# Optimization experiments

Hardware: AMD Instinct MI355X
Metric: run time of the kernel (lower is better)

The kernel has to match this reference:

```python
import jax, jax.numpy as jnp
import numpy as np

H, W = 1024, 2048
PS, ST = 16, 8          # patch_size, stride (init kwargs)
MARGIN = 1e-4           # margin from nerfstudio depth_ranking_loss
NH = (H - PS) // ST + 1  # 127
NW = (W - PS) // ST + 1  # 255
P = NH * NW             # 32385 patches
N = PS * PS             # 256 pixels per patch


def setup_inputs() -> dict:
    key = jax.random.key(0)
    k1, k2, k3, k4 = jax.random.split(key, 4)
    pred = jax.random.normal(k1, (1, 1, H, W), dtype=jnp.float32)
    target = jax.random.normal(k2, (1, 1, H, W), dtype=jnp.float32)
    mask = jax.random.bernoulli(k3, 0.5, (1, 1, H, W))
    # per-patch randomness standing in for torch.randperm: argsort of this
    # noise restricted to valid pixels is a uniform random permutation of
    # the masked (valid) pixel list.
    perm_noise = jax.random.uniform(k4, (P, N), dtype=jnp.float32)
    return {"pred": pred, "target": target, "mask": mask, "perm_noise": perm_noise}


def _extract_patches(x):
    # x: [H, W] -> [P, N] overlapping PSxPS patches with stride ST (scan order)
    i0 = jnp.arange(0, H - PS + 1, ST)           # [NH]
    j0 = jnp.arange(0, W - PS + 1, ST)           # [NW]
    ii = i0[:, None] + jnp.arange(PS)[None, :]   # [NH, PS]
    jj = j0[:, None] + jnp.arange(PS)[None, :]   # [NW, PS]
    g = x[ii[:, None, :, None], jj[None, :, None, :]]  # [NH, NW, PS, PS]
    return g.reshape(P, N)


def reference(pred, target, mask, perm_noise):
    pp = _extract_patches(pred[0, 0])            # [P, N]
    tp = _extract_patches(target[0, 0])          # [P, N]
    mp = _extract_patches(mask[0, 0])            # [P, N] bool

    # rank of each valid pixel in scan order (torch: pred_patch[mask] ordering)
    rank = jnp.cumsum(mp.astype(jnp.int32), axis=1) - 1        # [P, N]
    # random permutation of valid pixels: valid pixels sorted by noise come first
    noise = jnp.where(mp, perm_noise, jnp.inf)
    order = jnp.argsort(noise, axis=1)                          # [P, N]
    # valid pixel with scan-rank r pairs with order[r] (a random valid pixel)
    partner = jnp.take_along_axis(order, jnp.clip(rank, 0, N - 1), axis=1)

    dt = tp - jnp.take_along_axis(tp, partner, axis=1)
    dp = pp - jnp.take_along_axis(pp, partner, axis=1) + MARGIN

    # depth_ranking_loss: penalize pairs whose signs disagree, loss = mean |dp|
    sel = mp & (jnp.sign(dt) != jnp.sign(dp))
    cnt = jnp.sum(sel, axis=1).astype(pp.dtype)                 # [P]
    patch_loss = jnp.sum(jnp.where(sel, jnp.abs(dp), 0.0), axis=1) / cnt

    has_valid = jnp.any(mp, axis=1)                             # skip empty-mask patches
    n_used = jnp.sum(has_valid).astype(pp.dtype)
    return jnp.sum(jnp.where(has_valid, patch_loss, 0.0)) / n_used
```

## Files before the change

### kernel.cpp

```cpp
#include <hip/hip_runtime.h>
#include <cstdint>

#define H 1024
#define W 2048
#define PS 16
#define ST 8
#define NHH ((H - PS) / ST + 1)
#define NWW ((W - PS) / ST + 1)
#define NPATCH (NHH * NWW)
#define NN 256
#define MARGIN 1e-4f
#define WPB 4
#define NSLOT 128
#define SLOT_STRIDE 8

#define WS_VALID_F 1024

#define DPP_I(old, src, ctrl, rmask, bmask, bc) \
    __builtin_amdgcn_update_dpp((old), (src), (ctrl), (rmask), (bmask), (bc))

__device__ __forceinline__ unsigned wave_iscan_u32(unsigned x) {
    int v = (int)x;
    v += DPP_I(0, v, 0x111, 0xF, 0xF, true);
    v += DPP_I(0, v, 0x112, 0xF, 0xF, true);
    v += DPP_I(0, v, 0x114, 0xF, 0xF, true);
    v += DPP_I(0, v, 0x118, 0xF, 0xF, true);
    v += DPP_I(0, v, 0x142, 0xA, 0xF, true);
    v += DPP_I(0, v, 0x143, 0xC, 0xF, true);
    return (unsigned)v;
}

__device__ __forceinline__ float wave_iscan_f32(float x) {
    float v = x;
#define STEPF(ctrl, rmask) \
    v += __int_as_float(DPP_I(0, __float_as_int(v), (ctrl), (rmask), 0xF, true));
    STEPF(0x111, 0xF) STEPF(0x112, 0xF) STEPF(0x114, 0xF) STEPF(0x118, 0xF)
    STEPF(0x142, 0xA) STEPF(0x143, 0xC)
#undef STEPF
    return v;
}

__device__ __forceinline__ int rank_of(const unsigned* __restrict__ slot,
                                       unsigned w, unsigned key) {
    const unsigned b = w >> 16;
    const unsigned e = w & 0xFFFFu;
    const unsigned n = e - b;
    const unsigned v0 = slot[b + 0];
    const unsigned v1 = slot[b + 1];
    const unsigned v2 = slot[b + 2];
    const unsigned v3 = slot[b + 3];
    int rk = (int)b;
    rk += (n > 0u && v0 < key);
    rk += (n > 1u && v1 < key);
    rk += (n > 2u && v2 < key);
    rk += (n > 3u && v3 < key);
    if (__builtin_expect(n > 4u, 0)) {
        for (unsigned j = b + 4; j < e; ++j) rk += (slot[j] < key);
    }
    return rk;
}

__global__ __launch_bounds__(256, 8) void patch_loss_kernel(
    const float* __restrict__ pred, const float* __restrict__ target,
    const void* __restrict__ mask, const float* __restrict__ noise,
    float* __restrict__ lossAcc, float* __restrict__ validAcc)
{
    __shared__ unsigned sHist[WPB][NN];
    __shared__ unsigned sSlot[WPB][NN + 4];
    __shared__ float2   sPair[WPB][NN];

    const int tid  = threadIdx.x;
    const int lane = tid & 63;
    const int wid  = tid >> 6;
    const int p = blockIdx.x * WPB + wid;
    if (p >= NPATCH) return;

    const int ih = p / NWW;
    const int iw = p - ih * NWW;
    const int e0  = lane << 2;
    const int row = e0 >> 4;
    const int col = e0 & 15;
    const int pix = (ih * ST + row) * W + iw * ST + col;

    const float4 nz = *(const float4*)(noise + (size_t)p * NN + e0);

    const unsigned wb = *(const unsigned*)((const unsigned char*)mask + pix);
    int m0, m1, m2, m3;
    if (__ballot(wb > 1u) != 0ULL) {
        m0 = (wb & 0x000000FFu) != 0; m1 = (wb & 0x0000FF00u) != 0;
        m2 = (wb & 0x00FF0000u) != 0; m3 = (wb & 0xFF000000u) != 0;
    } else {
        const int4 mv = *(const int4*)((const int*)mask + pix);
        m0 = mv.x != 0; m1 = mv.y != 0; m2 = mv.z != 0; m3 = mv.w != 0;
    }

    const unsigned long long bl0 = __ballot(m0);
    const unsigned long long bl1 = __ballot(m1);
    const unsigned long long bl2 = __ballot(m2);
    const unsigned long long bl3 = __ballot(m3);
    const unsigned long long below = (1ULL << lane) - 1ULL;
    const int pre = __popcll(bl0 & below) + __popcll(bl1 & below)
                  + __popcll(bl2 & below) + __popcll(bl3 & below);
    const int cnt = __popcll(bl0) + __popcll(bl1)
                  + __popcll(bl2) + __popcll(bl3);
    const int r0 = pre;
    const int r1 = r0 + m0;
    const int r2 = r1 + m1;
    const int r3 = r2 + m2;

    const unsigned k0 = ((__float_as_uint(nz.x + 1.0f) - 0x3F800000u) << 8) | (unsigned)(e0 + 0);
    const unsigned k1 = ((__float_as_uint(nz.y + 1.0f) - 0x3F800000u) << 8) | (unsigned)(e0 + 1);
    const unsigned k2 = ((__float_as_uint(nz.z + 1.0f) - 0x3F800000u) << 8) | (unsigned)(e0 + 2);
    const unsigned k3 = ((__float_as_uint(nz.w + 1.0f) - 0x3F800000u) << 8) | (unsigned)(e0 + 3);

    *(uint4*)&sHist[wid][e0] = make_uint4(0u, 0u, 0u, 0u);
    __builtin_amdgcn_wave_barrier();
    if (m0) atomicAdd(&sHist[wid][k0 >> 23], 1u);
    if (m1) atomicAdd(&sHist[wid][k1 >> 23], 1u);
    if (m2) atomicAdd(&sHist[wid][k2 >> 23], 1u);
    if (m3) atomicAdd(&sHist[wid][k3 >> 23], 1u);
    __builtin_amdgcn_wave_barrier();

    const uint4 hq = *(uint4*)&sHist[wid][e0];
    const unsigned lsum = hq.x + hq.y + hq.z + hq.w;
    const unsigned hincl = wave_iscan_u32(lsum);
    const unsigned c0 = hincl - lsum;
    const unsigned c1 = c0 + hq.x;
    const unsigned c2 = c1 + hq.y;
    const unsigned c3 = c2 + hq.z;
    *(uint4*)&sHist[wid][e0] = make_uint4((c0 << 16) | c0, (c1 << 16) | c1,
                                          (c2 << 16) | c2, (c3 << 16) | c3);
    __builtin_amdgcn_wave_barrier();

    if (m0) { const unsigned s = atomicAdd(&sHist[wid][k0 >> 23], 1u) & 0xFFFFu; sSlot[wid][s] = k0; }
    if (m1) { const unsigned s = atomicAdd(&sHist[wid][k1 >> 23], 1u) & 0xFFFFu; sSlot[wid][s] = k1; }
    if (m2) { const unsigned s = atomicAdd(&sHist[wid][k2 >> 23], 1u) & 0xFFFFu; sSlot[wid][s] = k2; }
    if (m3) { const unsigned s = atomicAdd(&sHist[wid][k3 >> 23], 1u) & 0xFFFFu; sSlot[wid][s] = k3; }
    __builtin_amdgcn_wave_barrier();

    const float4 pv = *(const float4*)(pred + pix);
    const float4 tv = *(const float4*)(target + pix);

    const unsigned* __restrict__ slot  = sSlot[wid];
    const unsigned* __restrict__ histp = sHist[wid];
    const unsigned w0 = histp[k0 >> 23];
    const unsigned w1 = histp[k1 >> 23];
    const unsigned w2 = histp[k2 >> 23];
    const unsigned w3 = histp[k3 >> 23];
    const int rk0 = rank_of(slot, w0, k0);
    const int rk1 = rank_of(slot, w1, k1);
    const int rk2 = rank_of(slot, w2, k2);
    const int rk3 = rank_of(slot, w3, k3);

    if (m0) sPair[wid][rk0] = make_float2(tv.x, pv.x);
    if (m1) sPair[wid][rk1] = make_float2(tv.y, pv.y);
    if (m2) sPair[wid][rk2] = make_float2(tv.z, pv.z);
    if (m3) sPair[wid][rk3] = make_float2(tv.w, pv.w);
    __builtin_amdgcn_wave_barrier();

    const float2 q0 = sPair[wid][r0 & 255];
    const float2 q1 = sPair[wid][r1 & 255];
    const float2 q2 = sPair[wid][r2 & 255];
    const float2 q3 = sPair[wid][r3 & 255];

    float la = 0.0f;
    int   lc = 0;
    {
        const float dt = tv.x - q0.x, dp = pv.x - q0.y + MARGIN;
        const bool sel = m0 && (((dt > 0.0f) - (dt < 0.0f)) != ((dp > 0.0f) - (dp < 0.0f)));
        la += sel ? fabsf(dp) : 0.0f; lc += sel;
    }
    {
        const float dt = tv.y - q1.x, dp = pv.y - q1.y + MARGIN;
        const bool sel = m1 && (((dt > 0.0f) - (dt < 0.0f)) != ((dp > 0.0f) - (dp < 0.0f)));
        la += sel ? fabsf(dp) : 0.0f; lc += sel;
    }
    {
        const float dt = tv.z - q2.x, dp = pv.z - q2.y + MARGIN;
        const bool sel = m2 && (((dt > 0.0f) - (dt < 0.0f)) != ((dp > 0.0f) - (dp < 0.0f)));
        la += sel ? fabsf(dp) : 0.0f; lc += sel;
    }
    {
        const float dt = tv.w - q3.x, dp = pv.w - q3.y + MARGIN;
        const bool sel = m3 && (((dt > 0.0f) - (dt < 0.0f)) != ((dp > 0.0f) - (dp < 0.0f)));
        la += sel ? fabsf(dp) : 0.0f; lc += sel;
    }

    la = wave_iscan_f32(la);
    const unsigned lct = wave_iscan_u32((unsigned)lc);
    if (lane == 63 && cnt > 0) {
        const int slot_o = (p & (NSLOT - 1)) * SLOT_STRIDE;
        atomicAdd(&lossAcc[slot_o],  la / (float)lct);
        atomicAdd(&validAcc[slot_o], 1.0f);
    }
}

__global__ void finalize_kernel(const float* __restrict__ wsf,
                                float* __restrict__ out) {
    const int lane = threadIdx.x;
    float a = wsf[lane * SLOT_STRIDE] + wsf[(lane + 64) * SLOT_STRIDE];
    float b = wsf[WS_VALID_F + lane * SLOT_STRIDE]
            + wsf[WS_VALID_F + (lane + 64) * SLOT_STRIDE];
#pragma unroll
    for (int off = 32; off > 0; off >>= 1) {
        a += __shfl_down(a, off);
        b += __shfl_down(b, off);
    }
    if (lane == 0) out[0] = a / b;
}

extern "C" void kernel_launch(void* const* d_in, const int* in_sizes, int n_in,
                              void* d_out, int out_size, void* d_ws, size_t ws_size,
                              hipStream_t stream) {
    const float* pred   = (const float*)d_in[0];
    const float* target = (const float*)d_in[1];
    const void*  mask   = d_in[2];
    const float* noise  = (const float*)d_in[3];

    float* wsf      = (float*)d_ws;
    float* lossAcc  = wsf;
    float* validAcc = wsf + WS_VALID_F;

    const int nblocks = (NPATCH + WPB - 1) / WPB;
    patch_loss_kernel<<<nblocks, 256, 0, stream>>>(pred, target, mask, noise,
                                                   lossAcc, validAcc);
    finalize_kernel<<<1, 64, 0, stream>>>(wsf, (float*)d_out);
}
```

Before: 104.6 us.

## Invert pairing direction and use fixed-capacity bucket slots to drop a scatter pass

```diff
diff --git a/kernel.cpp b/kernel.cpp
--- a/kernel.cpp
+++ b/kernel.cpp
@@ -9,6 +9,8 @@
 #define NWW ((W - PS) / ST + 1)
 #define NPATCH (NHH * NWW)
 #define NN 256
+#define NBIN 256
+#define CAP 4
 #define MARGIN 1e-4f
 #define WPB 4
 #define NSLOT 128
@@ -40,33 +42,22 @@
     return v;
 }
 
-__device__ __forceinline__ int rank_of(const unsigned* __restrict__ slot,
-                                       unsigned w, unsigned key) {
-    const unsigned b = w >> 16;
-    const unsigned e = w & 0xFFFFu;
-    const unsigned n = e - b;
-    const unsigned v0 = slot[b + 0];
-    const unsigned v1 = slot[b + 1];
-    const unsigned v2 = slot[b + 2];
-    const unsigned v3 = slot[b + 3];
-    int rk = (int)b;
-    rk += (n > 0u && v0 < key);
-    rk += (n > 1u && v1 < key);
-    rk += (n > 2u && v2 < key);
-    rk += (n > 3u && v3 < key);
-    if (__builtin_expect(n > 4u, 0)) {
-        for (unsigned j = b + 4; j < e; ++j) rk += (slot[j] < key);
-    }
-    return rk;
-}
-
-__global__ __launch_bounds__(256, 8) void patch_loss_kernel(
+__device__ __forceinline__ int rank_in(uint4 c, unsigned n, unsigned key) {
+    int r = 0;
+    r += (n > 0u && c.x < key);
+    r += (n > 1u && c.y < key);
+    r += (n > 2u && c.z < key);
+    r += (n > 3u && c.w < key);
+    return r;
+}
+
+__global__ __launch_bounds__(256, 5) void patch_loss_kernel(
     const float* __restrict__ pred, const float* __restrict__ target,
     const void* __restrict__ mask, const float* __restrict__ noise,
     float* __restrict__ lossAcc, float* __restrict__ validAcc)
 {
-    __shared__ unsigned sHist[WPB][NN];
-    __shared__ unsigned sSlot[WPB][NN + 4];
+    __shared__ unsigned sHist[WPB][NBIN];
+    __shared__ unsigned sSlot[WPB][NBIN * CAP];
     __shared__ float2   sPair[WPB][NN];
 
     const int tid  = threadIdx.x;
@@ -82,7 +73,12 @@
     const int col = e0 & 15;
     const int pix = (ih * ST + row) * W + iw * ST + col;
 
+    *(uint4*)&sHist[wid][e0] = make_uint4(0u, 0u, 0u, 0u);
+    __builtin_amdgcn_wave_barrier();
+
     const float4 nz = *(const float4*)(noise + (size_t)p * NN + e0);
+    const float4 pv = *(const float4*)(pred + pix);
+    const float4 tv = *(const float4*)(target + pix);
 
     const unsigned wb = *(const unsigned*)((const unsigned char*)mask + pix);
     int m0, m1, m2, m3;
@@ -113,12 +109,19 @@
     const unsigned k2 = ((__float_as_uint(nz.z + 1.0f) - 0x3F800000u) << 8) | (unsigned)(e0 + 2);
     const unsigned k3 = ((__float_as_uint(nz.w + 1.0f) - 0x3F800000u) << 8) | (unsigned)(e0 + 3);
 
-    *(uint4*)&sHist[wid][e0] = make_uint4(0u, 0u, 0u, 0u);
-    __builtin_amdgcn_wave_barrier();
-    if (m0) atomicAdd(&sHist[wid][k0 >> 23], 1u);
-    if (m1) atomicAdd(&sHist[wid][k1 >> 23], 1u);
-    if (m2) atomicAdd(&sHist[wid][k2 >> 23], 1u);
-    if (m3) atomicAdd(&sHist[wid][k3 >> 23], 1u);
+    if (m0) sPair[wid][r0] = make_float2(tv.x, pv.x);
+    if (m1) sPair[wid][r1] = make_float2(tv.y, pv.y);
+    if (m2) sPair[wid][r2] = make_float2(tv.z, pv.z);
+    if (m3) sPair[wid][r3] = make_float2(tv.w, pv.w);
+
+    if (m0) { const unsigned a = atomicAdd(&sHist[wid][k0 >> 23], 1u);
+              if (a < CAP) sSlot[wid][((k0 >> 23) << 2) + a] = k0; }
+    if (m1) { const unsigned a = atomicAdd(&sHist[wid][k1 >> 23], 1u);
+              if (a < CAP) sSlot[wid][((k1 >> 23) << 2) + a] = k1; }
+    if (m2) { const unsigned a = atomicAdd(&sHist[wid][k2 >> 23], 1u);
+              if (a < CAP) sSlot[wid][((k2 >> 23) << 2) + a] = k2; }
+    if (m3) { const unsigned a = atomicAdd(&sHist[wid][k3 >> 23], 1u);
+              if (a < CAP) sSlot[wid][((k3 >> 23) << 2) + a] = k3; }
     __builtin_amdgcn_wave_barrier();
 
     const uint4 hq = *(uint4*)&sHist[wid][e0];
@@ -128,60 +131,47 @@
     const unsigned c1 = c0 + hq.x;
     const unsigned c2 = c1 + hq.y;
     const unsigned c3 = c2 + hq.z;
-    *(uint4*)&sHist[wid][e0] = make_uint4((c0 << 16) | c0, (c1 << 16) | c1,
-                                          (c2 << 16) | c2, (c3 << 16) | c3);
+    *(uint4*)&sHist[wid][e0] = make_uint4((c0 << 16) | hq.x, (c1 << 16) | hq.y,
+                                          (c2 << 16) | hq.z, (c3 << 16) | hq.w);
     __builtin_amdgcn_wave_barrier();
 
-    if (m0) { const unsigned s = atomicAdd(&sHist[wid][k0 >> 23], 1u) & 0xFFFFu; sSlot[wid][s] = k0; }
-    if (m1) { const unsigned s = atomicAdd(&sHist[wid][k1 >> 23], 1u) & 0xFFFFu; sSlot[wid][s] = k1; }
-    if (m2) { const unsigned s = atomicAdd(&sHist[wid][k2 >> 23], 1u) & 0xFFFFu; sSlot[wid][s] = k2; }
-    if (m3) { const unsigned s = atomicAdd(&sHist[wid][k3 >> 23], 1u) & 0xFFFFu; sSlot[wid][s] = k3; }
-    __builtin_amdgcn_wave_barrier();
-
-    const float4 pv = *(const float4*)(pred + pix);
-    const float4 tv = *(const float4*)(target + pix);
-
-    const unsigned* __restrict__ slot  = sSlot[wid];
-    const unsigned* __restrict__ histp = sHist[wid];
-    const unsigned w0 = histp[k0 >> 23];
-    const unsigned w1 = histp[k1 >> 23];
-    const unsigned w2 = histp[k2 >> 23];
-    const unsigned w3 = histp[k3 >> 23];
-    const int rk0 = rank_of(slot, w0, k0);
-    const int rk1 = rank_of(slot, w1, k1);
-    const int rk2 = rank_of(slot, w2, k2);
-    const int rk3 = rank_of(slot, w3, k3);
-
-    if (m0) sPair[wid][rk0] = make_float2(tv.x, pv.x);
-    if (m1) sPair[wid][rk1] = make_float2(tv.y, pv.y);
-    if (m2) sPair[wid][rk2] = make_float2(tv.z, pv.z);
-    if (m3) sPair[wid][rk3] = make_float2(tv.w, pv.w);
-    __builtin_amdgcn_wave_barrier();
-
-    const float2 q0 = sPair[wid][r0 & 255];
-    const float2 q1 = sPair[wid][r1 & 255];
-    const float2 q2 = sPair[wid][r2 & 255];
-    const float2 q3 = sPair[wid][r3 & 255];
+    const unsigned w0 = sHist[wid][k0 >> 23];
+    const unsigned w1 = sHist[wid][k1 >> 23];
+    const unsigned w2 = sHist[wid][k2 >> 23];
+    const unsigned w3 = sHist[wid][k3 >> 23];
+    const uint4 cd0 = *(const uint4*)&sSlot[wid][(k0 >> 23) << 2];
+    const uint4 cd1 = *(const uint4*)&sSlot[wid][(k1 >> 23) << 2];
+    const uint4 cd2 = *(const uint4*)&sSlot[wid][(k2 >> 23) << 2];
+    const uint4 cd3 = *(const uint4*)&sSlot[wid][(k3 >> 23) << 2];
+    const int rk0 = (int)(w0 >> 16) + rank_in(cd0, w0 & 0xFFFFu, k0);
+    const int rk1 = (int)(w1 >> 16) + rank_in(cd1, w1 & 0xFFFFu, k1);
+    const int rk2 = (int)(w2 >> 16) + rank_in(cd2, w2 & 0xFFFFu, k2);
+    const int rk3 = (int)(w3 >> 16) + rank_in(cd3, w3 & 0xFFFFu, k3);
+
+    const float2 q0 = sPair[wid][rk0 & 255];
+    const float2 q1 = sPair[wid][rk1 & 255];
+    const float2 q2 = sPair[wid][rk2 & 255];
+    const float2 q3 = sPair[wid][rk3 & 255];
 
     float la = 0.0f;
     int   lc = 0;
     {
-        const float dt = tv.x - q0.x, dp = pv.x - q0.y + MARGIN;
+        const float dt = q0.x - tv.x, dp = q0.y - pv.x + MARGIN;
         const bool sel = m0 && (((dt > 0.0f) - (dt < 0.0f)) != ((dp > 0.0f) - (dp < 0.0f)));
         la += sel ? fabsf(dp) : 0.0f; lc += sel;
     }
     {
-        const float dt = tv.y - q1.x, dp = pv.y - q1.y + MARGIN;
+        const float dt = q1.x - tv.y, dp = q1.y - pv.y + MARGIN;
         const bool sel = m1 && (((dt > 0.0f) - (dt < 0.0f)) != ((dp > 0.0f) - (dp < 0.0f)));
         la += sel ? fabsf(dp) : 0.0f; lc += sel;
     }
     {
-        const float dt = tv.z - q2.x, dp = pv.z - q2.y + MARGIN;
+        const float dt = q2.x - tv.z, dp = q2.y - pv.z + MARGIN;
         const bool sel = m2 && (((dt > 0.0f) - (dt < 0.0f)) != ((dp > 0.0f) - (dp < 0.0f)));
         la += sel ? fabsf(dp) : 0.0f; lc += sel;
     }
     {
-        const float dt = tv.w - q3.x, dp = pv.w - q3.y + MARGIN;
+        const float dt = q3.x - tv.w, dp = q3.y - pv.w + MARGIN;
         const bool sel = m3 && (((dt > 0.0f) - (dt < 0.0f)) != ((dp > 0.0f) - (dp < 0.0f)));
         la += sel ? fabsf(dp) : 0.0f; lc += sel;
     }
```

New measurement: 107.1 us. +2.4%, slower.
